# Kernel optimization log

Measured on AMD Instinct MI355X. Metric: run time of the kernel, lower is better.

## Reference

```python
import jax, jax.numpy as jnp
import numpy as np

BIG = 3.4028234e+38  # torch fill value used as additive mask
EPS = 1e-5           # nn.LayerNorm default eps


def _layernorm(x):
    mu = jnp.mean(x, axis=-1, keepdims=True)
    var = jnp.mean(jnp.square(x - mu), axis=-1, keepdims=True)
    return (x - mu) / jnp.sqrt(var + EPS)


def setup_inputs() -> dict:
    key = jax.random.key(0)
    ks = jax.random.split(key, 12)
    B, N, H, S = 32, 512, 256, 3  # batch, num_codes, embedding_size, num_stacks
    features = jax.random.normal(ks[0], (B, N, H), dtype=jnp.float32)
    masks = jnp.ones((B, N, 1), dtype=jnp.float32)
    guide = jax.random.randint(ks[1], (B, N, N), 0, 2).astype(jnp.float32)
    prior_guide = jax.random.uniform(ks[2], (B, N, N), dtype=jnp.float32)
    sc = 0.02
    WQ = jax.random.normal(ks[3], (S, H, H), dtype=jnp.float32) * sc
    WK = jax.random.normal(ks[4], (S, H, H), dtype=jnp.float32) * sc
    WV = jax.random.normal(ks[5], (S, H, H), dtype=jnp.float32) * sc
    W1 = jax.random.normal(ks[6], (S, H, H), dtype=jnp.float32) * sc
    b1 = jnp.zeros((S, H), dtype=jnp.float32)
    W2 = jax.random.normal(ks[7], (S, H, H), dtype=jnp.float32) * sc
    b2 = jnp.zeros((S, H), dtype=jnp.float32)
    return {"features": features, "masks": masks, "guide": guide,
            "prior_guide": prior_guide, "WQ": WQ, "WK": WK, "WV": WV,
            "W1": W1, "b1": b1, "W2": W2, "b2": b2}


def reference(features, masks, guide, prior_guide, WQ, WK, WV, W1, b1, W2, b2):
    H = features.shape[-1]
    scale = 1.0 / jnp.sqrt(jnp.float32(H))
    attention_mask = jnp.where(masks[:, :, 0] != 0, 0.0, BIG)  # [B,N]
    inf_mask = jnp.where(guide != 0, 0.0, BIG)                 # [B,N,N]
    attentions = []
    x = features
    for i in range(WQ.shape[0]):
        f = masks * x                                          # [B,N,H]
        if i == 0:
            att = prior_guide[:, None, :, :]                   # use_prior path
        else:
            q = jnp.einsum('bnh,hd->bnd', f, WQ[i].T)          # nn.Linear: x @ W^T
            k = jnp.einsum('bnh,hd->bnd', f, WK[i].T)
            pre = jnp.einsum('bqd,bkd->bqk', q, k) * scale     # [B,N,N] (heads=1)
            pre = pre - attention_mask[:, None, :] - inf_mask
            att = jax.nn.softmax(pre, axis=-1)[:, None, :, :]  # [B,1,N,N]
        attentions.append(att)
        v = jnp.einsum('bnh,hd->bnd', f, WV[i].T)              # [B,N,H]
        post = jnp.einsum('bqk,bkh->bqh', att[:, 0], v)        # squeeze head dim
        post = _layernorm(post + f)
        ffn = jnp.maximum(jnp.einsum('bnh,hd->bnd', post, W1[i].T) + b1[i], 0.0)
        ffn = jnp.einsum('bnh,hd->bnd', ffn, W2[i].T) + b2[i]
        x = _layernorm(ffn + post)
    return x * masks, jnp.stack(attentions)
```

## Files before the change

### kernel.cpp

```cpp
#include <hip/hip_runtime.h>
#include <cstdint>
#include <cstddef>

#define B_ 32
#define N_ 512
#define H_ 256
#define S_ 3
#define BN_ (B_*N_)
#define HH_ (H_*H_)
#define BIGF 3.4028234e+38f
#define EPSF 1e-5f

typedef __bf16 bf16x8 __attribute__((ext_vector_type(8)));
typedef float  f32x4  __attribute__((ext_vector_type(4)));

typedef const void __attribute__((address_space(1)))* gas_t;
typedef void __attribute__((address_space(3)))* las_t;

__device__ __forceinline__ void async16(const unsigned short* g, unsigned short* l) {
  __builtin_amdgcn_global_load_lds((gas_t)g, (las_t)l, 16, 0, 0);
}

__device__ __forceinline__ unsigned short f2bf(float f) {
  __bf16 h = (__bf16)f;
  unsigned short s;
  __builtin_memcpy(&s, &h, 2);
  return s;
}
__device__ __forceinline__ float bf2f(unsigned short u) {
  unsigned int v = ((unsigned int)u) << 16;
  float f;
  __builtin_memcpy(&f, &v, 4);
  return f;
}

#define KC_STAGE(lane) ((((lane) & 3) ^ (((lane) >> 3) & 3)) * 8)
#define KC_READ(quad, l15) ((((quad) ^ (((l15) >> 1) & 3))) * 8)

__global__ __launch_bounds__(256) void cvt_all_k(
    const float* __restrict__ WQ, const float* __restrict__ WK,
    const float* __restrict__ WV, const float* __restrict__ W1,
    const float* __restrict__ W2,
    unsigned short* __restrict__ wqk, unsigned short* __restrict__ wv,
    unsigned short* __restrict__ w1, unsigned short* __restrict__ w2) {
  const int per = S_ * HH_ / 4;
  int gi = blockIdx.x * 256 + threadIdx.x;
  int which = gi / per;
  int e4 = gi - which * per;
  float4 v;
  if      (which == 0) v = ((const float4*)WQ)[e4];
  else if (which == 1) v = ((const float4*)WK)[e4];
  else if (which == 2) v = ((const float4*)WV)[e4];
  else if (which == 3) v = ((const float4*)W1)[e4];
  else                 v = ((const float4*)W2)[e4];
  ushort4 o;
  o.x = f2bf(v.x); o.y = f2bf(v.y); o.z = f2bf(v.z); o.w = f2bf(v.w);
  int e = e4 * 4;
  if (which <= 1) {
    int L = e / HH_, off = e - L * HH_;
    *(ushort4*)&wqk[(size_t)L * 2 * HH_ + (which == 1 ? HH_ : 0) + off] = o;
  } else if (which == 2) ((ushort4*)wv)[e4] = o;
  else if   (which == 3) ((ushort4*)w1)[e4] = o;
  else                   ((ushort4*)w2)[e4] = o;
}

__global__ __launch_bounds__(256) void mask_mul_k(
    const float* __restrict__ x, const float* __restrict__ masks,
    unsigned short* __restrict__ fb) {
  int i = blockIdx.x * 256 + threadIdx.x;
  int row = i >> 6;
  float m = masks[row];
  float4 v = ((const float4*)x)[i];
  ushort4 o;
  o.x = f2bf(v.x * m); o.y = f2bf(v.y * m); o.z = f2bf(v.z * m); o.w = f2bf(v.w * m);
  ((ushort4*)fb)[i] = o;
}

__global__ __launch_bounds__(256) void mfma_gemm_k(
    const unsigned short* __restrict__ A, const unsigned short* __restrict__ Bm,
    unsigned short* __restrict__ Cb,
    int K, int Nn, int lda, int ldb, long sA, long sB, long sC) {
  __shared__ __align__(16) unsigned short As[128 * 32];
  __shared__ __align__(16) unsigned short Bs[128 * 32];
  const int b = blockIdx.z;
  const int t = threadIdx.x;
  const int wave = t >> 6, lane = t & 63;
  const int wm = wave >> 1, wn = wave & 1;
  const int quad = lane >> 4, l15 = lane & 15;
  const int m0 = blockIdx.y * 128, n0 = blockIdx.x * 128;
  const int srow = lane >> 2;
  const int kc = KC_STAGE(lane);
  const int pos8 = (lane & 3) * 8;

  const unsigned short* pa0 = A + (size_t)b * sA + (size_t)(m0 + wave * 32 + srow) * lda + kc;
  const unsigned short* pa1 = pa0 + 16 * (size_t)lda;
  const unsigned short* pb0 = Bm + (size_t)b * sB + (size_t)(n0 + wave * 32 + srow) * ldb + kc;
  const unsigned short* pb1 = pb0 + 16 * (size_t)ldb;
  unsigned short* la0 = &As[(wave * 32 + srow) * 32 + pos8];
  unsigned short* la1 = la0 + 16 * 32;
  unsigned short* lb0 = &Bs[(wave * 32 + srow) * 32 + pos8];
  unsigned short* lb1 = lb0 + 16 * 32;

  f32x4 acc[4][4];
#pragma unroll
  for (int i = 0; i < 4; ++i)
#pragma unroll
    for (int j = 0; j < 4; ++j) acc[i][j] = (f32x4){0.f, 0.f, 0.f, 0.f};

  const int soff = KC_READ(quad, l15);
  for (int k0 = 0; k0 < K; k0 += 32) {
    async16(pa0 + k0, la0); async16(pa1 + k0, la1);
    async16(pb0 + k0, lb0); async16(pb1 + k0, lb1);
    __syncthreads();
    bf16x8 af[4], bfr[4];
#pragma unroll
    for (int i = 0; i < 4; ++i)
      af[i] = *(const bf16x8*)&As[(wm * 64 + i * 16 + l15) * 32 + soff];
#pragma unroll
    for (int j = 0; j < 4; ++j)
      bfr[j] = *(const bf16x8*)&Bs[(wn * 64 + j * 16 + l15) * 32 + soff];
#pragma unroll
    for (int i = 0; i < 4; ++i)
#pragma unroll
      for (int j = 0; j < 4; ++j)
        acc[i][j] = __builtin_amdgcn_mfma_f32_16x16x32_bf16(af[i], bfr[j], acc[i][j], 0, 0, 0);
    __syncthreads();
  }

#pragma unroll
  for (int i = 0; i < 4; ++i) {
    const int rbase = m0 + wm * 64 + i * 16 + quad * 4;
#pragma unroll
    for (int j = 0; j < 4; ++j) {
      const int c = n0 + wn * 64 + j * 16 + l15;
#pragma unroll
      for (int r = 0; r < 4; ++r)
        Cb[(size_t)b * sC + (size_t)(rbase + r) * Nn + c] = f2bf(acc[i][j][r]);
    }
  }
}

template<int PRIOR>
__global__ __launch_bounds__(512) void ls_pv_k(
    const unsigned short* __restrict__ qk, const float* __restrict__ prior,
    const float* __restrict__ masks, const float* __restrict__ guide,
    const unsigned short* __restrict__ vT, const unsigned short* __restrict__ resb,
    float* __restrict__ att, float* __restrict__ post, unsigned short* __restrict__ postb) {
  __shared__ __align__(16) unsigned short As[64 * 32];
  __shared__ __align__(16) unsigned short Bs[512 * 32];
  __shared__ __align__(16) unsigned short Ps[64 * 520];
  __shared__ float red[4][64][2];
  const int b = blockIdx.z;
  const int t = threadIdx.x;
  const int wave = t >> 6, lane = t & 63;
  const int quad = lane >> 4, l15 = lane & 15;
  const int m0 = blockIdx.y * 64;
  const int srow = lane >> 2;
  const int kc = KC_STAGE(lane);
  const int pos8 = (lane & 3) * 8;
  const int soff = KC_READ(quad, l15);

  if (PRIOR) {
    const float* src = prior + ((size_t)b * N_ + m0) * N_;
    float*       dst = att   + ((size_t)b * N_ + m0) * N_;
#pragma unroll
    for (int s = 0; s < 16; ++s) {
      int idx4 = s * 512 + t;
      float4 v = ((const float4*)src)[idx4];
      ((float4*)dst)[idx4] = v;
      int row = idx4 >> 7, col4 = idx4 & 127;
      ushort4 o;
      o.x = f2bf(v.x); o.y = f2bf(v.y); o.z = f2bf(v.z); o.w = f2bf(v.w);
      *(ushort4*)&Ps[row * 520 + col4 * 4] = o;
    }
    __syncthreads();
  } else {
    const int wm = wave >> 2, wn = wave & 3;
    const int ld = 2 * H_;
    const unsigned short* base = qk + (size_t)b * N_ * ld;
    const unsigned short* pa = base + (size_t)(m0 + wave * 16 + srow) * ld + kc;
    unsigned short* la = &As[(wave * 16 + srow) * 32 + pos8];
    const unsigned short* pb = base + H_ + (size_t)(wave * 64 + srow) * ld + kc;
    unsigned short* lb = &Bs[(wave * 64 + srow) * 32 + pos8];

    f32x4 acc[2][8];
#pragma unroll
    for (int i = 0; i < 2; ++i)
#pragma unroll
      for (int j = 0; j < 8; ++j) acc[i][j] = (f32x4){0.f, 0.f, 0.f, 0.f};

    for (int k0 = 0; k0 < H_; k0 += 32) {
      if (wave < 4) async16(pa + k0, la);
#pragma unroll
      for (int c = 0; c < 4; ++c)
        async16(pb + (size_t)c * 16 * ld + k0, lb + c * 16 * 32);
      __syncthreads();
      bf16x8 af[2], bfr[8];
#pragma unroll
      for (int i = 0; i < 2; ++i)
        af[i] = *(const bf16x8*)&As[(wm * 32 + i * 16 + l15) * 32 + soff];
#pragma unroll
      for (int j = 0; j < 8; ++j)
        bfr[j] = *(const bf16x8*)&Bs[(wn * 128 + j * 16 + l15) * 32 + soff];
#pragma unroll
      for (int i = 0; i < 2; ++i)
#pragma unroll
        for (int j = 0; j < 8; ++j)
          acc[i][j] = __builtin_amdgcn_mfma_f32_16x16x32_bf16(af[i], bfr[j], acc[i][j], 0, 0, 0);
      __syncthreads();
    }

    float am[8];
#pragma unroll
    for (int j = 0; j < 8; ++j) {
      float mv = masks[(size_t)b * N_ + wn * 128 + j * 16 + l15];
      am[j] = (mv != 0.f) ? 0.f : BIGF;
    }
#pragma unroll
    for (int i = 0; i < 2; ++i) {
#pragma unroll
      for (int r = 0; r < 4; ++r) {
        const int mloc = wm * 32 + i * 16 + quad * 4 + r;
        const float* gr = guide + ((size_t)b * N_ + m0 + mloc) * N_;
        float mx = -BIGF;
#pragma unroll
        for (int j = 0; j < 8; ++j) {
          const int c = wn * 128 + j * 16 + l15;
          float g = gr[c];
          float v = acc[i][j][r] * 0.0625f - am[j] - ((g != 0.f) ? 0.f : BIGF);
          acc[i][j][r] = v;
          mx = fmaxf(mx, v);
        }
#pragma unroll
        for (int off = 1; off < 16; off <<= 1) mx = fmaxf(mx, __shfl_xor(mx, off));
        if (l15 == 0) red[wn][mloc][0] = mx;
      }
    }
    __syncthreads();
#pragma unroll
    for (int i = 0; i < 2; ++i) {
#pragma unroll
      for (int r = 0; r < 4; ++r) {
        const int mloc = wm * 32 + i * 16 + quad * 4 + r;
        float M = fmaxf(fmaxf(red[0][mloc][0], red[1][mloc][0]),
                        fmaxf(red[2][mloc][0], red[3][mloc][0]));
        float s = 0.f;
#pragma unroll
        for (int j = 0; j < 8; ++j) {
          float e = __expf(acc[i][j][r] - M);
          acc[i][j][r] = e;
          s += e;
        }
#pragma unroll
        for (int off = 1; off < 16; off <<= 1) s += __shfl_xor(s, off);
        if (l15 == 0) red[wn][mloc][1] = s;
      }
    }
    __syncthreads();
#pragma unroll
    for (int i = 0; i < 2; ++i) {
#pragma unroll
      for (int r = 0; r < 4; ++r) {
        const int mloc = wm * 32 + i * 16 + quad * 4 + r;
        float S = red[0][mloc][1] + red[1][mloc][1] + red[2][mloc][1] + red[3][mloc][1];
        float inv = 1.f / S;
        const size_t rowoff = ((size_t)b * N_ + m0 + mloc) * N_;
#pragma unroll
        for (int j = 0; j < 8; ++j) {
          const int c = wn * 128 + j * 16 + l15;
          float o = acc[i][j][r] * inv;
          att[rowoff + c] = o;
          Ps[mloc * 520 + c] = f2bf(o);
        }
      }
    }
    __syncthreads();
  }

  const int wm2 = wave >> 2, wn2 = wave & 3;
  const unsigned short* vb = vT + (size_t)b * H_ * N_;
  const unsigned short* pv0 = vb + (size_t)(wave * 16 + srow) * N_ + kc;
  const unsigned short* pv1 = pv0 + (size_t)128 * N_;
  unsigned short* lv0 = &Bs[(wave * 16 + srow) * 32 + pos8];
  unsigned short* lv1 = lv0 + 128 * 32;

  f32x4 acc2[2][4];
#pragma unroll
  for (int i = 0; i < 2; ++i)
#pragma unroll
    for (int j = 0; j < 4; ++j) acc2[i][j] = (f32x4){0.f, 0.f, 0.f, 0.f};

  for (int k0 = 0; k0 < N_; k0 += 32) {
    async16(pv0 + k0, lv0);
    async16(pv1 + k0, lv1);
    __syncthreads();
    bf16x8 af[2], bfr[4];
#pragma unroll
    for (int i = 0; i < 2; ++i)
      af[i] = *(const bf16x8*)&Ps[(wm2 * 32 + i * 16 + l15) * 520 + k0 + quad * 8];
#pragma unroll
    for (int j = 0; j < 4; ++j)
      bfr[j] = *(const bf16x8*)&Bs[(wn2 * 64 + j * 16 + l15) * 32 + soff];
#pragma unroll
    for (int i = 0; i < 2; ++i)
#pragma unroll
      for (int j = 0; j < 4; ++j)
        acc2[i][j] = __builtin_amdgcn_mfma_f32_16x16x32_bf16(af[i], bfr[j], acc2[i][j], 0, 0, 0);
    __syncthreads();
  }

#pragma unroll
  for (int i = 0; i < 2; ++i) {
#pragma unroll
    for (int r = 0; r < 4; ++r) {
      const int mloc = wm2 * 32 + i * 16 + quad * 4 + r;
      const long grow = (long)b * N_ + m0 + mloc;
      float s = 0.f, q = 0.f;
#pragma unroll
      for (int j = 0; j < 4; ++j) {
        const int c = wn2 * 64 + j * 16 + l15;
        float v = acc2[i][j][r] + bf2f(resb[grow * H_ + c]);
        acc2[i][j][r] = v;
        s += v; q += v * v;
      }
#pragma unroll
      for (int off = 1; off < 16; off <<= 1) {
        s += __shfl_xor(s, off);
        q += __shfl_xor(q, off);
      }
      if (l15 == 0) { red[wn2][mloc][0] = s; red[wn2][mloc][1] = q; }
    }
  }
  __syncthreads();
#pragma unroll
  for (int i = 0; i < 2; ++i) {
#pragma unroll
    for (int r = 0; r < 4; ++r) {
      const int mloc = wm2 * 32 + i * 16 + quad * 4 + r;
      const long grow = (long)b * N_ + m0 + mloc;
      float S = red[0][mloc][0] + red[1][mloc][0] + red[2][mloc][0] + red[3][mloc][0];
      float Q = red[0][mloc][1] + red[1][mloc][1] + red[2][mloc][1] + red[3][mloc][1];
      float mu = S * (1.f / H_);
      float var = Q * (1.f / H_) - mu * mu;
      float inv = 1.f / sqrtf(var + EPSF);
#pragma unroll
      for (int j = 0; j < 4; ++j) {
        const int c = wn2 * 64 + j * 16 + l15;
        float o = (acc2[i][j][r] - mu) * inv;
        post[grow * H_ + c] = o;
        postb[grow * H_ + c] = f2bf(o);
      }
    }
  }
}

template<int LAST>
__global__ __launch_bounds__(512) void ffn_k(
    const unsigned short* __restrict__ postb, const float* __restrict__ postf,
    const unsigned short* __restrict__ w1, const float* __restrict__ b1,
    const unsigned short* __restrict__ w2, const float* __restrict__ b2,
    const float* __restrict__ masks,
    unsigned short* __restrict__ fb, float* __restrict__ outx) {
  __shared__ __align__(16) unsigned short As[64 * 32];
  __shared__ __align__(16) unsigned short Bs[256 * 32];
  __shared__ __align__(16) unsigned short T1[64 * 264];
  __shared__ float red[4][64][2];
  const int t = threadIdx.x;
  const int wave = t >> 6, lane = t & 63;
  const int wm = wave >> 2, wn = wave & 3;
  const int quad = lane >> 4, l15 = lane & 15;
  const int m0 = blockIdx.y * 64;
  const int srow = lane >> 2;
  const int kc = KC_STAGE(lane);
  const int pos8 = (lane & 3) * 8;
  const int soff = KC_READ(quad, l15);

  const unsigned short* pa = postb + (size_t)(m0 + wave * 16 + srow) * H_ + kc;
  unsigned short* la = &As[(wave * 16 + srow) * 32 + pos8];
  unsigned short* lb0 = &Bs[(wave * 16 + srow) * 32 + pos8];
  unsigned short* lb1 = lb0 + 128 * 32;

  {
    const unsigned short* pb0 = w1 + (size_t)(wave * 16 + srow) * H_ + kc;
    const unsigned short* pb1 = pb0 + (size_t)128 * H_;
    f32x4 acc[2][4];
#pragma unroll
    for (int i = 0; i < 2; ++i)
#pragma unroll
      for (int j = 0; j < 4; ++j) acc[i][j] = (f32x4){0.f, 0.f, 0.f, 0.f};
    for (int k0 = 0; k0 < H_; k0 += 32) {
      if (wave < 4) async16(pa + k0, la);
      async16(pb0 + k0, lb0);
      async16(pb1 + k0, lb1);
      __syncthreads();
      bf16x8 af[2], bfr[4];
#pragma unroll
      for (int i = 0; i < 2; ++i)
        af[i] = *(const bf16x8*)&As[(wm * 32 + i * 16 + l15) * 32 + soff];
#pragma unroll
      for (int j = 0; j < 4; ++j)
        bfr[j] = *(const bf16x8*)&Bs[(wn * 64 + j * 16 + l15) * 32 + soff];
#pragma unroll
      for (int i = 0; i < 2; ++i)
#pragma unroll
        for (int j = 0; j < 4; ++j)
          acc[i][j] = __builtin_amdgcn_mfma_f32_16x16x32_bf16(af[i], bfr[j], acc[i][j], 0, 0, 0);
      __syncthreads();
    }
    float bv[4];
#pragma unroll
    for (int j = 0; j < 4; ++j) bv[j] = b1[wn * 64 + j * 16 + l15];
#pragma unroll
    for (int i = 0; i < 2; ++i) {
#pragma unroll
      for (int r = 0; r < 4; ++r) {
        const int mloc = wm * 32 + i * 16 + quad * 4 + r;
#pragma unroll
        for (int j = 0; j < 4; ++j) {
          const int c = wn * 64 + j * 16 + l15;
          T1[mloc * 264 + c] = f2bf(fmaxf(acc[i][j][r] + bv[j], 0.f));
        }
      }
    }
  }
  __syncthreads();

  {
    const unsigned short* pb0 = w2 + (size_t)(wave * 16 + srow) * H_ + kc;
    const unsigned short* pb1 = pb0 + (size_t)128 * H_;
    f32x4 acc[2][4];
#pragma unroll
    for (int i = 0; i < 2; ++i)
#pragma unroll
      for (int j = 0; j < 4; ++j) acc[i][j] = (f32x4){0.f, 0.f, 0.f, 0.f};
    for (int k0 = 0; k0 < H_; k0 += 32) {
      async16(pb0 + k0, lb0);
      async16(pb1 + k0, lb1);
      __syncthreads();
      bf16x8 af[2], bfr[4];
#pragma unroll
      for (int i = 0; i < 2; ++i)
        af[i] = *(const bf16x8*)&T1[(wm * 32 + i * 16 + l15) * 264 + k0 + quad * 8];
#pragma unroll
      for (int j = 0; j < 4; ++j)
        bfr[j] = *(const bf16x8*)&Bs[(wn * 64 + j * 16 + l15) * 32 + soff];
#pragma unroll
      for (int i = 0; i < 2; ++i)
#pragma unroll
        for (int j = 0; j < 4; ++j)
          acc[i][j] = __builtin_amdgcn_mfma_f32_16x16x32_bf16(af[i], bfr[j], acc[i][j], 0, 0, 0);
      __syncthreads();
    }
    float bv[4];
#pragma unroll
    for (int j = 0; j < 4; ++j) bv[j] = b2[wn * 64 + j * 16 + l15];
#pragma unroll
    for (int i = 0; i < 2; ++i) {
#pragma unroll
      for (int r = 0; r < 4; ++r) {
        const int mloc = wm * 32 + i * 16 + quad * 4 + r;
        const long grow = (long)m0 + mloc;
        float s = 0.f, q = 0.f;
#pragma unroll
        for (int j = 0; j < 4; ++j) {
          const int c = wn * 64 + j * 16 + l15;
          float v = acc[i][j][r] + bv[j] + postf[grow * H_ + c];
          acc[i][j][r] = v;
          s += v; q += v * v;
        }
#pragma unroll
        for (int off = 1; off < 16; off <<= 1) {
          s += __shfl_xor(s, off);
          q += __shfl_xor(q, off);
        }
        if (l15 == 0) { red[wn][mloc][0] = s; red[wn][mloc][1] = q; }
      }
    }
    __syncthreads();
#pragma unroll
    for (int i = 0; i < 2; ++i) {
#pragma unroll
      for (int r = 0; r < 4; ++r) {
        const int mloc = wm * 32 + i * 16 + quad * 4 + r;
        const long grow = (long)m0 + mloc;
        float S = red[0][mloc][0] + red[1][mloc][0] + red[2][mloc][0] + red[3][mloc][0];
        float Q = red[0][mloc][1] + red[1][mloc][1] + red[2][mloc][1] + red[3][mloc][1];
        float mu = S * (1.f / H_);
        float var = Q * (1.f / H_) - mu * mu;
        float inv = 1.f / sqrtf(var + EPSF);
        float mval = masks[grow];
#pragma unroll
        for (int j = 0; j < 4; ++j) {
          const int c = wn * 64 + j * 16 + l15;
          float o = (acc[i][j][r] - mu) * inv * mval;
          if (LAST) outx[grow * H_ + c] = o;
          else      fb[grow * H_ + c] = f2bf(o);
        }
      }
    }
  }
}

extern "C" void kernel_launch(void* const* d_in, const int* in_sizes, int n_in,
                              void* d_out, int out_size, void* d_ws, size_t ws_size,
                              hipStream_t stream) {
  const float* features = (const float*)d_in[0];
  const float* masks    = (const float*)d_in[1];
  const float* guide    = (const float*)d_in[2];
  const float* prior    = (const float*)d_in[3];
  const float* WQ       = (const float*)d_in[4];
  const float* WK       = (const float*)d_in[5];
  const float* WV       = (const float*)d_in[6];
  const float* W1       = (const float*)d_in[7];
  const float* b1       = (const float*)d_in[8];
  const float* W2       = (const float*)d_in[9];
  const float* b2       = (const float*)d_in[10];

  float* out     = (float*)d_out;
  float* out_x   = out;
  float* out_att = out + (size_t)BN_ * H_;

  char* w = (char*)d_ws;
  float* post = (float*)w;                     w += (size_t)BN_ * H_ * 4;
  unsigned short* f_bf   = (unsigned short*)w; w += (size_t)BN_ * H_ * 2;
  unsigned short* qk_bf  = (unsigned short*)w; w += (size_t)BN_ * 2 * H_ * 2;
  unsigned short* post_bf= (unsigned short*)w; w += (size_t)BN_ * H_ * 2;
  unsigned short* vT     = (unsigned short*)w; w += (size_t)BN_ * H_ * 2;
  unsigned short* wqk_bf = (unsigned short*)w; w += (size_t)S_ * 2 * HH_ * 2;
  unsigned short* wv_bf  = (unsigned short*)w; w += (size_t)S_ * HH_ * 2;
  unsigned short* w1_bf  = (unsigned short*)w; w += (size_t)S_ * HH_ * 2;
  unsigned short* w2_bf  = (unsigned short*)w; w += (size_t)S_ * HH_ * 2;

  dim3 g_cvt(5 * S_ * HH_ / 1024);
  dim3 g_ew(BN_ * H_ / 1024);
  dim3 g_qkp(4, BN_ / 128, 1);
  dim3 g_vt(4, 2, B_);
  dim3 g_ls(1, N_ / 64, B_);
  dim3 g_ffn(1, BN_ / 64, 1);

  cvt_all_k<<<g_cvt, 256, 0, stream>>>(WQ, WK, WV, W1, W2, wqk_bf, wv_bf, w1_bf, w2_bf);
  mask_mul_k<<<g_ew, 256, 0, stream>>>(features, masks, f_bf);

  const long sF  = (long)N_ * H_;
  const long sVT = (long)H_ * N_;

  for (int i = 0; i < S_; ++i) {
    float* att = out_att + (size_t)i * B_ * N_ * N_;
    mfma_gemm_k<<<g_vt, 256, 0, stream>>>(wv_bf + (size_t)i * HH_, f_bf, vT,
                                          H_, N_, H_, H_, 0, sF, sVT);
    if (i == 0) {
      ls_pv_k<1><<<g_ls, 512, 0, stream>>>(nullptr, prior, nullptr, nullptr,
                                           vT, f_bf, att, post, post_bf);
    } else {
      mfma_gemm_k<<<g_qkp, 256, 0, stream>>>(f_bf, wqk_bf + (size_t)i * 2 * HH_, qk_bf,
                                             H_, 2 * H_, H_, H_, 0, 0, 0);
      ls_pv_k<0><<<g_ls, 512, 0, stream>>>(qk_bf, nullptr, masks, guide,
                                           vT, f_bf, att, post, post_bf);
    }
    if (i < S_ - 1) {
      ffn_k<0><<<g_ffn, 512, 0, stream>>>(post_bf, post,
          w1_bf + (size_t)i * HH_, b1 + (size_t)i * H_,
          w2_bf + (size_t)i * HH_, b2 + (size_t)i * H_, masks, f_bf, nullptr);
    } else {
      ffn_k<1><<<g_ffn, 512, 0, stream>>>(post_bf, post,
          w1_bf + (size_t)i * HH_, b1 + (size_t)i * H_,
          w2_bf + (size_t)i * HH_, b2 + (size_t)i * H_, masks, nullptr, out_x);
    }
  }
}
```

Baseline: 403.6 us.

## Double-buffer LDS tiles and prefetch next-stage operands across all GEMM kernels

Converts the K-loops of the generic GEMM, the attention/PV kernel and the FFN kernel to double-buffered LDS staging, issuing the async global-to-LDS loads for the next K tile before computing on the current one. The first V or W2 tile is also prefetched before the softmax or ReLU epilogue so that latency is hidden behind it. The attention grid is reordered so batch is on blockIdx.x. This roughly doubles LDS use per block, which may lower occupancy in the already LDS-heavy attention kernel.

After: 377.8 us. -6.4%, faster.

```diff
diff --git a/kernel.cpp b/kernel.cpp
--- a/kernel.cpp
+++ b/kernel.cpp
@@ -80,8 +80,8 @@
     const unsigned short* __restrict__ A, const unsigned short* __restrict__ Bm,
     unsigned short* __restrict__ Cb,
     int K, int Nn, int lda, int ldb, long sA, long sB, long sC) {
-  __shared__ __align__(16) unsigned short As[128 * 32];
-  __shared__ __align__(16) unsigned short Bs[128 * 32];
+  __shared__ __align__(16) unsigned short As[2][128 * 32];
+  __shared__ __align__(16) unsigned short Bs[2][128 * 32];
   const int b = blockIdx.z;
   const int t = threadIdx.x;
   const int wave = t >> 6, lane = t & 63;
@@ -96,10 +96,7 @@
   const unsigned short* pa1 = pa0 + 16 * (size_t)lda;
   const unsigned short* pb0 = Bm + (size_t)b * sB + (size_t)(n0 + wave * 32 + srow) * ldb + kc;
   const unsigned short* pb1 = pb0 + 16 * (size_t)ldb;
-  unsigned short* la0 = &As[(wave * 32 + srow) * 32 + pos8];
-  unsigned short* la1 = la0 + 16 * 32;
-  unsigned short* lb0 = &Bs[(wave * 32 + srow) * 32 + pos8];
-  unsigned short* lb1 = lb0 + 16 * 32;
+  const int lo = (wave * 32 + srow) * 32 + pos8;
 
   f32x4 acc[4][4];
 #pragma unroll
@@ -108,23 +105,31 @@
     for (int j = 0; j < 4; ++j) acc[i][j] = (f32x4){0.f, 0.f, 0.f, 0.f};
 
   const int soff = KC_READ(quad, l15);
-  for (int k0 = 0; k0 < K; k0 += 32) {
-    async16(pa0 + k0, la0); async16(pa1 + k0, la1);
-    async16(pb0 + k0, lb0); async16(pb1 + k0, lb1);
-    __syncthreads();
+  const int NT = K >> 5;
+  async16(pa0, &As[0][lo]); async16(pa1, &As[0][lo + 16 * 32]);
+  async16(pb0, &Bs[0][lo]); async16(pb1, &Bs[0][lo + 16 * 32]);
+  __syncthreads();
+  int cur = 0;
+  for (int tt = 0; tt < NT; ++tt) {
+    if (tt + 1 < NT) {
+      const int kn = (tt + 1) << 5;
+      async16(pa0 + kn, &As[cur ^ 1][lo]); async16(pa1 + kn, &As[cur ^ 1][lo + 16 * 32]);
+      async16(pb0 + kn, &Bs[cur ^ 1][lo]); async16(pb1 + kn, &Bs[cur ^ 1][lo + 16 * 32]);
+    }
     bf16x8 af[4], bfr[4];
 #pragma unroll
     for (int i = 0; i < 4; ++i)
-      af[i] = *(const bf16x8*)&As[(wm * 64 + i * 16 + l15) * 32 + soff];
+      af[i] = *(const bf16x8*)&As[cur][(wm * 64 + i * 16 + l15) * 32 + soff];
 #pragma unroll
     for (int j = 0; j < 4; ++j)
-      bfr[j] = *(const bf16x8*)&Bs[(wn * 64 + j * 16 + l15) * 32 + soff];
+      bfr[j] = *(const bf16x8*)&Bs[cur][(wn * 64 + j * 16 + l15) * 32 + soff];
 #pragma unroll
     for (int i = 0; i < 4; ++i)
 #pragma unroll
       for (int j = 0; j < 4; ++j)
         acc[i][j] = __builtin_amdgcn_mfma_f32_16x16x32_bf16(af[i], bfr[j], acc[i][j], 0, 0, 0);
     __syncthreads();
+    cur ^= 1;
   }
 
 #pragma unroll
@@ -146,11 +151,11 @@
     const float* __restrict__ masks, const float* __restrict__ guide,
     const unsigned short* __restrict__ vT, const unsigned short* __restrict__ resb,
     float* __restrict__ att, float* __restrict__ post, unsigned short* __restrict__ postb) {
-  __shared__ __align__(16) unsigned short As[64 * 32];
-  __shared__ __align__(16) unsigned short Bs[512 * 32];
+  __shared__ __align__(16) unsigned short As[2][64 * 32];
+  __shared__ __align__(16) unsigned short Bs[2][512 * 32];
   __shared__ __align__(16) unsigned short Ps[64 * 520];
   __shared__ float red[4][64][2];
-  const int b = blockIdx.z;
+  const int b = blockIdx.x;
   const int t = threadIdx.x;
   const int wave = t >> 6, lane = t & 63;
   const int quad = lane >> 4, l15 = lane & 15;
@@ -160,7 +165,14 @@
   const int pos8 = (lane & 3) * 8;
   const int soff = KC_READ(quad, l15);
 
+  const unsigned short* vb = vT + (size_t)b * H_ * N_;
+  const unsigned short* pv0 = vb + (size_t)(wave * 16 + srow) * N_ + kc;
+  const unsigned short* pv1 = pv0 + (size_t)128 * N_;
+  const int lvo = (wave * 16 + srow) * 32 + pos8;
+
   if (PRIOR) {
+    async16(pv0, &Bs[0][lvo]);
+    async16(pv1, &Bs[0][lvo + 128 * 32]);
     const float* src = prior + ((size_t)b * N_ + m0) * N_;
     float*       dst = att   + ((size_t)b * N_ + m0) * N_;
 #pragma unroll
@@ -179,9 +191,9 @@
     const int ld = 2 * H_;
     const unsigned short* base = qk + (size_t)b * N_ * ld;
     const unsigned short* pa = base + (size_t)(m0 + wave * 16 + srow) * ld + kc;
-    unsigned short* la = &As[(wave * 16 + srow) * 32 + pos8];
     const unsigned short* pb = base + H_ + (size_t)(wave * 64 + srow) * ld + kc;
-    unsigned short* lb = &Bs[(wave * 64 + srow) * 32 + pos8];
+    const int lao = (wave * 16 + srow) * 32 + pos8;
+    const int lbo = (wave * 64 + srow) * 32 + pos8;
 
     f32x4 acc[2][8];
 #pragma unroll
@@ -189,26 +201,39 @@
 #pragma unroll
       for (int j = 0; j < 8; ++j) acc[i][j] = (f32x4){0.f, 0.f, 0.f, 0.f};
 
-    for (int k0 = 0; k0 < H_; k0 += 32) {
-      if (wave < 4) async16(pa + k0, la);
-#pragma unroll
-      for (int c = 0; c < 4; ++c)
-        async16(pb + (size_t)c * 16 * ld + k0, lb + c * 16 * 32);
-      __syncthreads();
+    if (wave < 4) async16(pa, &As[0][lao]);
+#pragma unroll
+    for (int c = 0; c < 4; ++c)
+      async16(pb + (size_t)c * 16 * ld, &Bs[0][lbo + c * 16 * 32]);
+    __syncthreads();
+    int cur = 0;
+#pragma unroll
+    for (int tt = 0; tt < 8; ++tt) {
+      if (tt < 7) {
+        const int kn = (tt + 1) * 32;
+        if (wave < 4) async16(pa + kn, &As[cur ^ 1][lao]);
+#pragma unroll
+        for (int c = 0; c < 4; ++c)
+          async16(pb + (size_t)c * 16 * ld + kn, &Bs[cur ^ 1][lbo + c * 16 * 32]);
+      }
       bf16x8 af[2], bfr[8];
 #pragma unroll
       for (int i = 0; i < 2; ++i)
-        af[i] = *(const bf16x8*)&As[(wm * 32 + i * 16 + l15) * 32 + soff];
+        af[i] = *(const bf16x8*)&As[cur][(wm * 32 + i * 16 + l15) * 32 + soff];
 #pragma unroll
       for (int j = 0; j < 8; ++j)
-        bfr[j] = *(const bf16x8*)&Bs[(wn * 128 + j * 16 + l15) * 32 + soff];
+        bfr[j] = *(const bf16x8*)&Bs[cur][(wn * 128 + j * 16 + l15) * 32 + soff];
 #pragma unroll
       for (int i = 0; i < 2; ++i)
 #pragma unroll
         for (int j = 0; j < 8; ++j)
           acc[i][j] = __builtin_amdgcn_mfma_f32_16x16x32_bf16(af[i], bfr[j], acc[i][j], 0, 0, 0);
       __syncthreads();
-    }
+      cur ^= 1;
+    }
+
+    async16(pv0, &Bs[0][lvo]);
+    async16(pv1, &Bs[0][lvo + 128 * 32]);
 
     float am[8];
 #pragma unroll
@@ -278,11 +303,6 @@
   }
 
   const int wm2 = wave >> 2, wn2 = wave & 3;
-  const unsigned short* vb = vT + (size_t)b * H_ * N_;
-  const unsigned short* pv0 = vb + (size_t)(wave * 16 + srow) * N_ + kc;
-  const unsigned short* pv1 = pv0 + (size_t)128 * N_;
-  unsigned short* lv0 = &Bs[(wave * 16 + srow) * 32 + pos8];
-  unsigned short* lv1 = lv0 + 128 * 32;
 
   f32x4 acc2[2][4];
 #pragma unroll
@@ -290,23 +310,28 @@
 #pragma unroll
     for (int j = 0; j < 4; ++j) acc2[i][j] = (f32x4){0.f, 0.f, 0.f, 0.f};
 
-  for (int k0 = 0; k0 < N_; k0 += 32) {
-    async16(pv0 + k0, lv0);
-    async16(pv1 + k0, lv1);
-    __syncthreads();
+  int cur = 0;
+#pragma unroll
+  for (int tt = 0; tt < 16; ++tt) {
+    if (tt < 15) {
+      const int kn = (tt + 1) * 32;
+      async16(pv0 + kn, &Bs[cur ^ 1][lvo]);
+      async16(pv1 + kn, &Bs[cur ^ 1][lvo + 128 * 32]);
+    }
     bf16x8 af[2], bfr[4];
 #pragma unroll
     for (int i = 0; i < 2; ++i)
-      af[i] = *(const bf16x8*)&Ps[(wm2 * 32 + i * 16 + l15) * 520 + k0 + quad * 8];
+      af[i] = *(const bf16x8*)&Ps[(wm2 * 32 + i * 16 + l15) * 520 + tt * 32 + quad * 8];
 #pragma unroll
     for (int j = 0; j < 4; ++j)
-      bfr[j] = *(const bf16x8*)&Bs[(wn2 * 64 + j * 16 + l15) * 32 + soff];
+      bfr[j] = *(const bf16x8*)&Bs[cur][(wn2 * 64 + j * 16 + l15) * 32 + soff];
 #pragma unroll
     for (int i = 0; i < 2; ++i)
 #pragma unroll
       for (int j = 0; j < 4; ++j)
         acc2[i][j] = __builtin_amdgcn_mfma_f32_16x16x32_bf16(af[i], bfr[j], acc2[i][j], 0, 0, 0);
     __syncthreads();
+    cur ^= 1;
   }
 
 #pragma unroll
@@ -361,8 +386,8 @@
     const unsigned short* __restrict__ w2, const float* __restrict__ b2,
     const float* __restrict__ masks,
     unsigned short* __restrict__ fb, float* __restrict__ outx) {
-  __shared__ __align__(16) unsigned short As[64 * 32];
-  __shared__ __align__(16) unsigned short Bs[256 * 32];
+  __shared__ __align__(16) unsigned short As[2][64 * 32];
+  __shared__ __align__(16) unsigned short Bs[2][256 * 32];
   __shared__ __align__(16) unsigned short T1[64 * 264];
   __shared__ float red[4][64][2];
   const int t = threadIdx.x;
@@ -376,9 +401,11 @@
   const int soff = KC_READ(quad, l15);
 
   const unsigned short* pa = postb + (size_t)(m0 + wave * 16 + srow) * H_ + kc;
-  unsigned short* la = &As[(wave * 16 + srow) * 32 + pos8];
-  unsigned short* lb0 = &Bs[(wave * 16 + srow) * 32 + pos8];
-  unsigned short* lb1 = lb0 + 128 * 32;
+  const int lao = (wave * 16 + srow) * 32 + pos8;
+  const int lbo = (wave * 16 + srow) * 32 + pos8;
+
+  const unsigned short* qb0 = w2 + (size_t)(wave * 16 + srow) * H_ + kc;
+  const unsigned short* qb1 = qb0 + (size_t)128 * H_;
 
   {
     const unsigned short* pb0 = w1 + (size_t)(wave * 16 + srow) * H_ + kc;
@@ -388,25 +415,38 @@
     for (int i = 0; i < 2; ++i)
 #pragma unroll
       for (int j = 0; j < 4; ++j) acc[i][j] = (f32x4){0.f, 0.f, 0.f, 0.f};
-    for (int k0 = 0; k0 < H_; k0 += 32) {
-      if (wave < 4) async16(pa + k0, la);
-      async16(pb0 + k0, lb0);
-      async16(pb1 + k0, lb1);
-      __syncthreads();
+    if (wave < 4) async16(pa, &As[0][lao]);
+    async16(pb0, &Bs[0][lbo]);
+    async16(pb1, &Bs[0][lbo + 128 * 32]);
+    __syncthreads();
+    int cur = 0;
+#pragma unroll
+    for (int tt = 0; tt < 8; ++tt) {
+      if (tt < 7) {
+        const int kn = (tt + 1) * 32;
+        if (wave < 4) async16(pa + kn, &As[cur ^ 1][lao]);
+        async16(pb0 + kn, &Bs[cur ^ 1][lbo]);
+        async16(pb1 + kn, &Bs[cur ^ 1][lbo + 128 * 32]);
+      }
       bf16x8 af[2], bfr[4];
 #pragma unroll
       for (int i = 0; i < 2; ++i)
-        af[i] = *(const bf16x8*)&As[(wm * 32 + i * 16 + l15) * 32 + soff];
+        af[i] = *(const bf16x8*)&As[cur][(wm * 32 + i * 16 + l15) * 32 + soff];
 #pragma unroll
       for (int j = 0; j < 4; ++j)
-        bfr[j] = *(const bf16x8*)&Bs[(wn * 64 + j * 16 + l15) * 32 + soff];
+        bfr[j] = *(const bf16x8*)&Bs[cur][(wn * 64 + j * 16 + l15) * 32 + soff];
 #pragma unroll
       for (int i = 0; i < 2; ++i)
 #pragma unroll
         for (int j = 0; j < 4; ++j)
           acc[i][j] = __builtin_amdgcn_mfma_f32_16x16x32_bf16(af[i], bfr[j], acc[i][j], 0, 0, 0);
       __syncthreads();
-    }
+      cur ^= 1;
+    }
+
+    async16(qb0, &Bs[0][lbo]);
+    async16(qb1, &Bs[0][lbo + 128 * 32]);
+
     float bv[4];
 #pragma unroll
     for (int j = 0; j < 4; ++j) bv[j] = b1[wn * 64 + j * 16 + l15];
@@ -426,30 +466,33 @@
   __syncthreads();
 
   {
-    const unsigned short* pb0 = w2 + (size_t)(wave * 16 + srow) * H_ + kc;
-    const unsigned short* pb1 = pb0 + (size_t)128 * H_;
     f32x4 acc[2][4];
 #pragma unroll
     for (int i = 0; i < 2; ++i)
 #pragma unroll
       for (int j = 0; j < 4; ++j) acc[i][j] = (f32x4){0.f, 0.f, 0.f, 0.f};
-    for (int k0 = 0; k0 < H_; k0 += 32) {
-      async16(pb0 + k0, lb0);
-      async16(pb1 + k0, lb1);
-      __syncthreads();
+    int cur = 0;
+#pragma unroll
+    for (int tt = 0; tt < 8; ++tt) {
+      if (tt < 7) {
+        const int kn = (tt + 1) * 32;
+        async16(qb0 + kn, &Bs[cur ^ 1][lbo]);
+        async16(qb1 + kn, &Bs[cur ^ 1][lbo + 128 * 32]);
+      }
       bf16x8 af[2], bfr[4];
 #pragma unroll
       for (int i = 0; i < 2; ++i)
-        af[i] = *(const bf16x8*)&T1[(wm * 32 + i * 16 + l15) * 264 + k0 + quad * 8];
+        af[i] = *(const bf16x8*)&T1[(wm * 32 + i * 16 + l15) * 264 + tt * 32 + quad * 8];
 #pragma unroll
       for (int j = 0; j < 4; ++j)
-        bfr[j] = *(const bf16x8*)&Bs[(wn * 64 + j * 16 + l15) * 32 + soff];
+        bfr[j] = *(const bf16x8*)&Bs[cur][(wn * 64 + j * 16 + l15) * 32 + soff];
 #pragma unroll
       for (int i = 0; i < 2; ++i)
 #pragma unroll
         for (int j = 0; j < 4; ++j)
           acc[i][j] = __builtin_amdgcn_mfma_f32_16x16x32_bf16(af[i], bfr[j], acc[i][j], 0, 0, 0);
       __syncthreads();
+      cur ^= 1;
     }
     float bv[4];
 #pragma unroll
@@ -535,7 +578,7 @@
   dim3 g_ew(BN_ * H_ / 1024);
   dim3 g_qkp(4, BN_ / 128, 1);
   dim3 g_vt(4, 2, B_);
-  dim3 g_ls(1, N_ / 64, B_);
+  dim3 g_ls(B_, N_ / 64, 1);
   dim3 g_ffn(1, BN_ / 64, 1);
 
   cvt_all_k<<<g_cvt, 256, 0, stream>>>(WQ, WK, WV, W1, W2, wqk_bf, wv_bf, w1_bf, w2_bf);
```
